# Kernel tuning notes

Hardware: AMD Instinct MI355X
Metric: run time of the kernel (lower is better)

The kernel has to match this reference:

```python
import jax, jax.numpy as jnp
import numpy as np
import math

D_MODEL = 1024
NUM_HEADS = 16
HEAD_DIM = D_MODEL // NUM_HEADS
EPS = 1e-6
ROPE_BASE = 10000.0


def _rope_cos_sin(seq_len, dim, dtype):
    inv_freq = 1.0 / (ROPE_BASE ** (jnp.arange(0, dim, 2, dtype=jnp.float32) / dim))
    t = jnp.arange(seq_len, dtype=jnp.float32)
    freqs = jnp.outer(t, inv_freq)                 # [s, dim/2]
    emb = jnp.concatenate([freqs, freqs], axis=-1)  # [s, dim]
    return jnp.cos(emb).astype(dtype), jnp.sin(emb).astype(dtype)


def _rotate_half(x):
    x1, x2 = jnp.split(x, 2, axis=-1)
    return jnp.concatenate([-x2, x1], axis=-1)


def setup_inputs() -> dict:
    key = jax.random.key(0)
    k1, k2, k3 = jax.random.split(key, 3)
    b, s = 2, 2048
    x = jax.random.normal(k1, (b, s, D_MODEL), dtype=jnp.float32)
    norm_w = jnp.ones((D_MODEL,), dtype=jnp.float32)
    qkv_w = jax.random.normal(k2, (3 * D_MODEL, D_MODEL), dtype=jnp.float32) * (1.0 / math.sqrt(D_MODEL))
    qkv_b = jnp.zeros((3 * D_MODEL,), dtype=jnp.float32)
    proj_w = jax.random.normal(k3, (D_MODEL, D_MODEL), dtype=jnp.float32) * (1.0 / math.sqrt(D_MODEL))
    proj_b = jnp.zeros((D_MODEL,), dtype=jnp.float32)
    return {"x": x, "norm_w": norm_w, "qkv_w": qkv_w, "qkv_b": qkv_b,
            "proj_w": proj_w, "proj_b": proj_b}


def reference(x, norm_w, qkv_w, qkv_b, proj_w, proj_b):
    b, s, d = x.shape
    # RMSNorm (pre-LN)
    xn = x * jax.lax.rsqrt(jnp.mean(x * x, axis=-1, keepdims=True) + EPS) * norm_w
    # Fused QKV
    qkv = jnp.einsum('bsd,ed->bse', xn, qkv_w) + qkv_b
    q, k, v = jnp.split(qkv, 3, axis=-1)
    # [b, h, s, hd]
    def shape(t):
        return t.reshape(b, s, NUM_HEADS, HEAD_DIM).transpose(0, 2, 1, 3)
    q, k, v = shape(q), shape(k), shape(v)
    # RoPE on head_dim
    cos, sin = _rope_cos_sin(s, HEAD_DIM, x.dtype)  # [s, hd]
    q = q * cos + _rotate_half(q) * sin
    k = k * cos + _rotate_half(k) * sin
    # Naive causal attention
    scale = 1.0 / math.sqrt(HEAD_DIM)
    scores = jnp.einsum('bhqd,bhkd->bhqk', q, k) * scale
    causal = jnp.tril(jnp.ones((s, s), dtype=bool))
    scores = jnp.where(causal, scores, -jnp.inf)
    attn = jax.nn.softmax(scores, axis=-1)
    y = jnp.einsum('bhqk,bhkd->bhqd', attn, v)
    y = y.transpose(0, 2, 1, 3).reshape(b, s, d)
    return jnp.einsum('bsd,ed->bse', y, proj_w) + proj_b
```

## Files before the change

### kernel.cpp

```cpp
#include <hip/hip_runtime.h>
#include <cstdint>
#include <cstddef>

#define NB 2
#define NS 2048
#define ND 1024
#define NH 16
#define HD 64
#define ROWS 4096
#define E3 3072

using bf16 = __bf16;
typedef __attribute__((ext_vector_type(4))) __bf16 bf16x4;
typedef __attribute__((ext_vector_type(8))) __bf16 bf16x8;
typedef __attribute__((ext_vector_type(4))) float f32x4;

__device__ __forceinline__ f32x4 mfma16(bf16x8 a, bf16x8 b, f32x4 c) {
    return __builtin_amdgcn_mfma_f32_16x16x32_bf16(a, b, c, 0, 0, 0);
}

__device__ __forceinline__ void gll16(const bf16* src, bf16* lds) {
    __builtin_amdgcn_global_load_lds(
        (const __attribute__((address_space(1))) void*)src,
        (__attribute__((address_space(3))) void*)lds, 16, 0, 0);
}

__global__ __launch_bounds__(256) void rope_table(float4* __restrict__ tab) {
    int idx = blockIdx.x * 256 + threadIdx.x;
    int s = idx >> 4, j = idx & 15;
    float f0 = powf(10000.0f, -(float)j * (1.0f / 32.0f));
    float f1 = powf(10000.0f, -(float)(j + 16) * (1.0f / 32.0f));
    float sn0, c0, sn1, c1;
    sincosf((float)s * f0, &sn0, &c0);
    sincosf((float)s * f1, &sn1, &c1);
    tab[idx] = make_float4(c0, sn0, c1, sn1);
}

__global__ __launch_bounds__(256) void cast_weights(const float* __restrict__ qkv_w,
                                                    const float* __restrict__ proj_w,
                                                    bf16* __restrict__ wq) {
    const int n1 = E3 * ND;
    int i = (blockIdx.x * 256 + threadIdx.x) * 4;
    const float* src = (i < n1) ? (qkv_w + i) : (proj_w + (i - n1));
    float4 v = *(const float4*)src;
    bf16x4 o;
    o[0] = (bf16)v.x; o[1] = (bf16)v.y; o[2] = (bf16)v.z; o[3] = (bf16)v.w;
    *(bf16x4*)(wq + i) = o;
}

__global__ __launch_bounds__(256) void rmsnorm_cast(const float* __restrict__ x,
                                                    const float* __restrict__ w,
                                                    bf16* __restrict__ xn) {
    int row = blockIdx.x;
    int tid = threadIdx.x;
    const float* xr = x + (size_t)row * ND;
    float4 v = ((const float4*)xr)[tid];
    float ss = v.x*v.x + v.y*v.y + v.z*v.z + v.w*v.w;
    #pragma unroll
    for (int m = 32; m >= 1; m >>= 1) ss += __shfl_xor(ss, m);
    __shared__ float wsum[4];
    if ((tid & 63) == 0) wsum[tid >> 6] = ss;
    __syncthreads();
    float total = wsum[0] + wsum[1] + wsum[2] + wsum[3];
    float scale = rsqrtf(total * (1.0f / ND) + 1e-6f);
    float4 wv = ((const float4*)w)[tid];
    bf16x4 o;
    o[0] = (bf16)(v.x * scale * wv.x);
    o[1] = (bf16)(v.y * scale * wv.y);
    o[2] = (bf16)(v.z * scale * wv.z);
    o[3] = (bf16)(v.w * scale * wv.w);
    ((bf16x4*)(xn + (size_t)row * ND))[tid] = o;
}

__global__ __launch_bounds__(256) void gemm_qkv_rope(const bf16* __restrict__ A,
                                                     const bf16* __restrict__ Bm,
                                                     const float* __restrict__ bias,
                                                     const float4* __restrict__ tab,
                                                     bf16* __restrict__ Qb,
                                                     bf16* __restrict__ Kb,
                                                     bf16* __restrict__ Vf) {
    const int K = ND;
    __shared__ bf16 Asm[128 * 32];
    __shared__ bf16 Bsm[128 * 32];
    const int tid = threadIdx.x;
    const int wave = tid >> 6, lane = tid & 63;
    const int quad = lane >> 4, l15 = lane & 15;
    const int row0 = blockIdx.x * 128, col0 = blockIdx.y * 128;
    const int wr = (wave >> 1) * 64, wc = (wave & 1) * 64;
    const int srow = lane >> 2;
    const int scol = (lane & 3) * 8;

    f32x4 acc[4][4] = {};

    for (int k0 = 0; k0 < K; k0 += 32) {
        #pragma unroll
        for (int i = 0; i < 2; ++i) {
            int r = wave * 32 + i * 16;
            gll16(A + (size_t)(row0 + r + srow) * K + k0 + scol, Asm + r * 32);
            gll16(Bm + (size_t)(col0 + r + srow) * K + k0 + scol, Bsm + r * 32);
        }
        __syncthreads();
        bf16x8 af[4], bff[4];
        #pragma unroll
        for (int t = 0; t < 4; ++t) {
            af[t]  = *(const bf16x8*)(Asm + (wr + t * 16 + l15) * 32 + quad * 8);
            bff[t] = *(const bf16x8*)(Bsm + (wc + t * 16 + l15) * 32 + quad * 8);
        }
        #pragma unroll
        for (int mt = 0; mt < 4; ++mt)
            #pragma unroll
            for (int nt = 0; nt < 4; ++nt)
                acc[mt][nt] = mfma16(af[mt], bff[nt], acc[mt][nt]);
        __syncthreads();
    }

    float bb[4];
    #pragma unroll
    for (int nt = 0; nt < 4; ++nt) bb[nt] = bias[col0 + wc + nt * 16 + l15];

    const int region = col0 >> 10;
    if (region == 2) {
        const int cv = col0 - 2048 + wc;
        const int h = cv >> 6;
        const int b = row0 >> 11;
        const int sloc = row0 & (NS - 1);
        const int kg0 = (sloc + wr) >> 5;
        bf16* vh = Vf + (size_t)(b * NH + h) * 131072;
        #pragma unroll
        for (int Gw = 0; Gw < 2; ++Gw) {
            #pragma unroll
            for (int nt = 0; nt < 4; ++nt) {
                bf16x8 vf8;
                #pragma unroll
                for (int r = 0; r < 4; ++r) {
                    vf8[r]     = (bf16)(acc[2 * Gw][nt][r] + bb[nt]);
                    vf8[4 + r] = (bf16)(acc[2 * Gw + 1][nt][r] + bb[nt]);
                }
                *(bf16x8*)(vh + ((size_t)(kg0 + Gw) * 4 + nt) * 512 + lane * 8) = vf8;
            }
        }
    } else {
        const float scale = (region == 0) ? 0.125f : 1.0f;
        bf16* Ob = (region == 0) ? Qb : Kb;
        const int h = ((col0 + wc) & 1023) >> 6;
        #pragma unroll
        for (int mt = 0; mt < 4; ++mt) {
            #pragma unroll
            for (int r = 0; r < 4; ++r) {
                int row = row0 + wr + mt * 16 + quad * 4 + r;
                int s = row & (NS - 1);
                int b = row >> 11;
                float4 cs = tab[s * 16 + l15];
                size_t obase = ((size_t)(b * NH + h) * NS + s) * 64;
                #pragma unroll
                for (int nt = 0; nt < 4; ++nt) {
                    float v  = acc[mt][nt][r] + bb[nt];
                    float vp = acc[mt][nt ^ 2][r] + bb[nt ^ 2];
                    float cc = (nt & 1) ? cs.z : cs.x;
                    float ss = (nt & 1) ? cs.w : cs.y;
                    float res = (nt < 2) ? (v * cc - vp * ss) : (v * cc + vp * ss);
                    Ob[obase + nt * 16 + l15] = (bf16)(res * scale);
                }
            }
        }
    }
}

__global__ __launch_bounds__(256) void gemm_proj(const bf16* __restrict__ A,
                                                 const bf16* __restrict__ Bm,
                                                 const float* __restrict__ bias,
                                                 float* __restrict__ C) {
    __shared__ bf16 Asm[128 * 32];
    __shared__ bf16 Bsm[64 * 32];
    const int tid = threadIdx.x;
    const int wave = tid >> 6, lane = tid & 63;
    const int quad = lane >> 4, l15 = lane & 15;
    const int row0 = blockIdx.x * 128, col0 = blockIdx.y * 64;
    const int wr = (wave >> 1) * 64, wc = (wave & 1) * 32;
    const int srow = lane >> 2;
    const int scol = (lane & 3) * 8;

    f32x4 acc[4][2] = {};

    for (int k0 = 0; k0 < ND; k0 += 32) {
        gll16(A + (size_t)(row0 + wave * 32 + srow) * ND + k0 + scol, Asm + (wave * 32) * 32);
        gll16(A + (size_t)(row0 + wave * 32 + 16 + srow) * ND + k0 + scol, Asm + (wave * 32 + 16) * 32);
        gll16(Bm + (size_t)(col0 + wave * 16 + srow) * ND + k0 + scol, Bsm + (wave * 16) * 32);
        __syncthreads();
        bf16x8 af[4], bff[2];
        #pragma unroll
        for (int t = 0; t < 4; ++t)
            af[t] = *(const bf16x8*)(Asm + (wr + t * 16 + l15) * 32 + quad * 8);
        #pragma unroll
        for (int t = 0; t < 2; ++t)
            bff[t] = *(const bf16x8*)(Bsm + (wc + t * 16 + l15) * 32 + quad * 8);
        #pragma unroll
        for (int mt = 0; mt < 4; ++mt)
            #pragma unroll
            for (int nt = 0; nt < 2; ++nt)
                acc[mt][nt] = mfma16(af[mt], bff[nt], acc[mt][nt]);
        __syncthreads();
    }

    #pragma unroll
    for (int nt = 0; nt < 2; ++nt) {
        int col = col0 + wc + nt * 16 + l15;
        float bv = bias[col];
        #pragma unroll
        for (int mt = 0; mt < 4; ++mt) {
            int row = row0 + wr + mt * 16 + quad * 4;
            #pragma unroll
            for (int r = 0; r < 4; ++r)
                C[(size_t)(row + r) * ND + col] = acc[mt][nt][r] + bv;
        }
    }
}

__global__ __launch_bounds__(256) void attn(const bf16* __restrict__ Q,
                                            const bf16* __restrict__ K,
                                            const bf16* __restrict__ Vf,
                                            bf16* __restrict__ Y) {
    __shared__ bf16 Ksm[2][8192];
    __shared__ bf16 Vsm[2][8192];
    int bid = blockIdx.x;
    int g = bid >> 5;
    int bh = bid & 31;
    int qt = (g < 8) ? (15 - g) : (g - 8);
    int tid = threadIdx.x;
    int wave = tid >> 6, lane = tid & 63;
    int quad = lane >> 4, l15 = lane & 15;
    int q0 = qt * 128 + wave * 32;
    const bf16* Qh = Q + (size_t)bh * NS * 64;
    const bf16* Kh = K + (size_t)bh * NS * 64;
    const float NEG_INF = -__builtin_inff();

    const int krow = wave * 8 + (lane >> 3);
    const int ksx  = (lane & 7) ^ (krow & 7);
    const bf16* sK = Kh + (size_t)krow * 64 + ksx * 8;
    const bf16* sV = Vf + (size_t)bh * 131072 + wave * 2048 + lane * 8;

    const bf16* pk0 = &Ksm[0][l15 * 64 + ((quad) ^ (l15 & 7)) * 8];
    const bf16* pk1 = &Ksm[0][l15 * 64 + ((4 + quad) ^ (l15 & 7)) * 8];
    const bf16* pvf = &Vsm[0][lane * 8];

    bf16x8 bq[2][2];
    #pragma unroll
    for (int t = 0; t < 2; ++t)
        #pragma unroll
        for (int hh = 0; hh < 2; ++hh)
            bq[t][hh] = *(const bf16x8*)(Qh + (size_t)(q0 + t * 16 + l15) * 64 + hh * 32 + quad * 8);

    f32x4 o[2][4] = {};
    float lsum[2] = {0.f, 0.f};

    auto stage = [&](int c, int par) {
        const int kb = c * 128;
        bf16* dK = &Ksm[par][wave * 512];
        bf16* dV = &Vsm[par][wave * 2048];
        #pragma unroll
        for (int i = 0; i < 4; ++i)
            gll16(sK + (size_t)(kb + i * 32) * 64, dK + i * 2048);
        #pragma unroll
        for (int nt = 0; nt < 4; ++nt)
            gll16(sV + (size_t)(kb >> 5) * 2048 + nt * 512, dV + nt * 512);
    };

    auto compute = [&](int cc, int par) {
        const int kb = cc * 128;
        const int pb = par * 8192;
        #pragma unroll
        for (int ksub = 0; ksub < 4; ++ksub) {
            const int kbs = kb + ksub * 32;
            if (kbs <= q0) {
                bf16x8 ak00 = *(const bf16x8*)(pk0 + pb + ksub * 2048);
                bf16x8 ak01 = *(const bf16x8*)(pk1 + pb + ksub * 2048);
                bf16x8 ak10 = *(const bf16x8*)(pk0 + pb + ksub * 2048 + 1024);
                bf16x8 ak11 = *(const bf16x8*)(pk1 + pb + ksub * 2048 + 1024);
                bf16x8 vf0 = *(const bf16x8*)(pvf + pb + ksub * 2048);
                bf16x8 vf1 = *(const bf16x8*)(pvf + pb + ksub * 2048 + 512);
                bf16x8 vf2 = *(const bf16x8*)(pvf + pb + ksub * 2048 + 1024);
                bf16x8 vf3 = *(const bf16x8*)(pvf + pb + ksub * 2048 + 1536);
                const bool masked = (kbs == q0);
                #pragma unroll
                for (int t = 0; t < 2; ++t) {
                    f32x4 sh0 = {}, sh1 = {};
                    sh0 = mfma16(ak00, bq[t][0], sh0);
                    sh0 = mfma16(ak01, bq[t][1], sh0);
                    sh1 = mfma16(ak10, bq[t][0], sh1);
                    sh1 = mfma16(ak11, bq[t][1], sh1);
                    if (masked) {
                        int qy = q0 + t * 16 + l15;
                        #pragma unroll
                        for (int r = 0; r < 4; ++r) {
                            if (kbs + quad * 4 + r > qy)      sh0[r] = NEG_INF;
                            if (kbs + 16 + quad * 4 + r > qy) sh1[r] = NEG_INF;
                        }
                    }
                    bf16x8 pa;
                    float ls = 0.f;
                    #pragma unroll
                    for (int j = 0; j < 4; ++j) {
                        float p0 = __expf(sh0[j]);
                        float p1 = __expf(sh1[j]);
                        ls += p0 + p1;
                        pa[j] = (bf16)p0;
                        pa[4 + j] = (bf16)p1;
                    }
                    lsum[t] += ls;
                    o[t][0] = mfma16(pa, vf0, o[t][0]);
                    o[t][1] = mfma16(pa, vf1, o[t][1]);
                    o[t][2] = mfma16(pa, vf2, o[t][2]);
                    o[t][3] = mfma16(pa, vf3, o[t][3]);
                }
            }
        }
    };

    const int ncb = qt + 1;
    stage(0, 0);
    __syncthreads();
    for (int c = 0; c < ncb; ++c) {
        const int par = c & 1;
        if (c + 1 < ncb) stage(c + 1, par ^ 1);
        compute(c, par);
        __syncthreads();
    }

    int b = bh >> 4, h = bh & 15;
    #pragma unroll
    for (int t = 0; t < 2; ++t) {
        float red = lsum[t];
        red += __shfl_xor(red, 16);
        red += __shfl_xor(red, 32);
        #pragma unroll
        for (int r = 0; r < 4; ++r) {
            float il = 1.0f / __shfl(red, quad * 4 + r);
            size_t row = (size_t)(b * NS + q0 + t * 16 + quad * 4 + r);
            #pragma unroll
            for (int nt = 0; nt < 4; ++nt)
                Y[row * ND + h * 64 + nt * 16 + l15] = (bf16)(o[t][nt][r] * il);
        }
    }
}

extern "C" void kernel_launch(void* const* d_in, const int* in_sizes, int n_in,
                              void* d_out, int out_size, void* d_ws, size_t ws_size,
                              hipStream_t stream) {
    const float* x      = (const float*)d_in[0];
    const float* norm_w = (const float*)d_in[1];
    const float* qkv_w  = (const float*)d_in[2];
    const float* qkv_b  = (const float*)d_in[3];
    const float* proj_w = (const float*)d_in[4];
    const float* proj_b = (const float*)d_in[5];
    float* out = (float*)d_out;

    char* ws = (char*)d_ws;
    size_t off = 0;
    bf16* xn    = (bf16*)(ws + off); off += (size_t)ROWS * ND * 2;
    bf16* wq    = (bf16*)(ws + off); off += (size_t)E3 * ND * 2;
    bf16* wp    = (bf16*)(ws + off); off += (size_t)ND * ND * 2;
    bf16* Qb    = (bf16*)(ws + off); off += (size_t)NB * NH * NS * HD * 2;
    bf16* Kb    = (bf16*)(ws + off); off += (size_t)NB * NH * NS * HD * 2;
    bf16* Vfrag = (bf16*)(ws + off); off += (size_t)NB * NH * HD * NS * 2;
    bf16* Y     = (bf16*)(ws + off); off += (size_t)ROWS * ND * 2;
    float4* tab = (float4*)(ws + off); off += (size_t)NS * 16 * sizeof(float4);

    rope_table<<<NS * 16 / 256, 256, 0, stream>>>(tab);
    cast_weights<<<(E3 * ND + ND * ND) / 1024, 256, 0, stream>>>(qkv_w, proj_w, wq);
    rmsnorm_cast<<<ROWS, 256, 0, stream>>>(x, norm_w, xn);
    gemm_qkv_rope<<<dim3(ROWS / 128, E3 / 128), 256, 0, stream>>>(xn, wq, qkv_b, tab, Qb, Kb, Vfrag);
    attn<<<NB * NH * (NS / 128), 256, 0, stream>>>(Qb, Kb, Vfrag, Y);
    gemm_proj<<<dim3(ROWS / 128, ND / 64), 256, 0, stream>>>(Y, wp, proj_b, out);
}
```

Measured before the change: 191.4 us.

## Merge prep kernels and stage Q/K and attention outputs through LDS for coalesced stores

Combines the rope table, weight cast and RMSNorm kernels into one launch with block-index branching, removing two launch gaps. The Q/K RoPE epilogue and the attention output epilogue now write per-wave tiles into shared memory, then emit 16-byte vector stores to global memory. Previously each lane wrote scattered 2-byte values. The LDS staging adds shared-memory traffic and reuses buffers that must be idle by then, relying on prior barriers and explicit waitcnts.

```diff
diff --git a/kernel.cpp b/kernel.cpp
--- a/kernel.cpp
+++ b/kernel.cpp
@@ -25,51 +25,52 @@
         (__attribute__((address_space(3))) void*)lds, 16, 0, 0);
 }
 
-__global__ __launch_bounds__(256) void rope_table(float4* __restrict__ tab) {
-    int idx = blockIdx.x * 256 + threadIdx.x;
-    int s = idx >> 4, j = idx & 15;
-    float f0 = powf(10000.0f, -(float)j * (1.0f / 32.0f));
-    float f1 = powf(10000.0f, -(float)(j + 16) * (1.0f / 32.0f));
-    float sn0, c0, sn1, c1;
-    sincosf((float)s * f0, &sn0, &c0);
-    sincosf((float)s * f1, &sn1, &c1);
-    tab[idx] = make_float4(c0, sn0, c1, sn1);
-}
-
-__global__ __launch_bounds__(256) void cast_weights(const float* __restrict__ qkv_w,
-                                                    const float* __restrict__ proj_w,
-                                                    bf16* __restrict__ wq) {
-    const int n1 = E3 * ND;
-    int i = (blockIdx.x * 256 + threadIdx.x) * 4;
-    const float* src = (i < n1) ? (qkv_w + i) : (proj_w + (i - n1));
-    float4 v = *(const float4*)src;
-    bf16x4 o;
-    o[0] = (bf16)v.x; o[1] = (bf16)v.y; o[2] = (bf16)v.z; o[3] = (bf16)v.w;
-    *(bf16x4*)(wq + i) = o;
-}
-
-__global__ __launch_bounds__(256) void rmsnorm_cast(const float* __restrict__ x,
-                                                    const float* __restrict__ w,
-                                                    bf16* __restrict__ xn) {
-    int row = blockIdx.x;
+__global__ __launch_bounds__(256) void prep(const float* __restrict__ qkv_w,
+                                            const float* __restrict__ proj_w,
+                                            const float* __restrict__ x,
+                                            const float* __restrict__ norm_w,
+                                            bf16* __restrict__ wq,
+                                            bf16* __restrict__ xn,
+                                            float4* __restrict__ tab) {
+    __shared__ float wsum[4];
+    int bid = blockIdx.x;
     int tid = threadIdx.x;
-    const float* xr = x + (size_t)row * ND;
-    float4 v = ((const float4*)xr)[tid];
-    float ss = v.x*v.x + v.y*v.y + v.z*v.z + v.w*v.w;
-    #pragma unroll
-    for (int m = 32; m >= 1; m >>= 1) ss += __shfl_xor(ss, m);
-    __shared__ float wsum[4];
-    if ((tid & 63) == 0) wsum[tid >> 6] = ss;
-    __syncthreads();
-    float total = wsum[0] + wsum[1] + wsum[2] + wsum[3];
-    float scale = rsqrtf(total * (1.0f / ND) + 1e-6f);
-    float4 wv = ((const float4*)w)[tid];
-    bf16x4 o;
-    o[0] = (bf16)(v.x * scale * wv.x);
-    o[1] = (bf16)(v.y * scale * wv.y);
-    o[2] = (bf16)(v.z * scale * wv.z);
-    o[3] = (bf16)(v.w * scale * wv.w);
-    ((bf16x4*)(xn + (size_t)row * ND))[tid] = o;
+    if (bid < 4096) {
+        const int n1 = E3 * ND;
+        int i = (bid * 256 + tid) * 4;
+        const float* src = (i < n1) ? (qkv_w + i) : (proj_w + (i - n1));
+        float4 v = *(const float4*)src;
+        bf16x4 o;
+        o[0] = (bf16)v.x; o[1] = (bf16)v.y; o[2] = (bf16)v.z; o[3] = (bf16)v.w;
+        *(bf16x4*)(wq + i) = o;
+    } else if (bid < 8192) {
+        int row = bid - 4096;
+        const float* xr = x + (size_t)row * ND;
+        float4 v = ((const float4*)xr)[tid];
+        float ss = v.x*v.x + v.y*v.y + v.z*v.z + v.w*v.w;
+        #pragma unroll
+        for (int m = 32; m >= 1; m >>= 1) ss += __shfl_xor(ss, m);
+        if ((tid & 63) == 0) wsum[tid >> 6] = ss;
+        __syncthreads();
+        float total = wsum[0] + wsum[1] + wsum[2] + wsum[3];
+        float scale = rsqrtf(total * (1.0f / ND) + 1e-6f);
+        float4 wv = ((const float4*)norm_w)[tid];
+        bf16x4 o;
+        o[0] = (bf16)(v.x * scale * wv.x);
+        o[1] = (bf16)(v.y * scale * wv.y);
+        o[2] = (bf16)(v.z * scale * wv.z);
+        o[3] = (bf16)(v.w * scale * wv.w);
+        ((bf16x4*)(xn + (size_t)row * ND))[tid] = o;
+    } else {
+        int idx = (bid - 8192) * 256 + tid;
+        int s = idx >> 4, j = idx & 15;
+        float f0 = powf(10000.0f, -(float)j * (1.0f / 32.0f));
+        float f1 = powf(10000.0f, -(float)(j + 16) * (1.0f / 32.0f));
+        float sn0, c0, sn1, c1;
+        sincosf((float)s * f0, &sn0, &c0);
+        sincosf((float)s * f1, &sn1, &c1);
+        tab[idx] = make_float4(c0, sn0, c1, sn1);
+    }
 }
 
 __global__ __launch_bounds__(256) void gemm_qkv_rope(const bf16* __restrict__ A,
@@ -80,8 +81,9 @@
                                                      bf16* __restrict__ Kb,
                                                      bf16* __restrict__ Vf) {
     const int K = ND;
-    __shared__ bf16 Asm[128 * 32];
-    __shared__ bf16 Bsm[128 * 32];
+    __shared__ bf16 smem[8192];
+    bf16* Asm = smem;
+    bf16* Bsm = smem + 4096;
     const int tid = threadIdx.x;
     const int wave = tid >> 6, lane = tid & 63;
     const int quad = lane >> 4, l15 = lane & 15;
@@ -143,25 +145,40 @@
         const float scale = (region == 0) ? 0.125f : 1.0f;
         bf16* Ob = (region == 0) ? Qb : Kb;
         const int h = ((col0 + wc) & 1023) >> 6;
-        #pragma unroll
-        for (int mt = 0; mt < 4; ++mt) {
-            #pragma unroll
-            for (int r = 0; r < 4; ++r) {
-                int row = row0 + wr + mt * 16 + quad * 4 + r;
-                int s = row & (NS - 1);
-                int b = row >> 11;
-                float4 cs = tab[s * 16 + l15];
-                size_t obase = ((size_t)(b * NH + h) * NS + s) * 64;
+        bf16* ep = smem + wave * 2048;
+        #pragma unroll
+        for (int p = 0; p < 2; ++p) {
+            #pragma unroll
+            for (int mtl = 0; mtl < 2; ++mtl) {
+                const int mt = p * 2 + mtl;
                 #pragma unroll
-                for (int nt = 0; nt < 4; ++nt) {
-                    float v  = acc[mt][nt][r] + bb[nt];
-                    float vp = acc[mt][nt ^ 2][r] + bb[nt ^ 2];
-                    float cc = (nt & 1) ? cs.z : cs.x;
-                    float ss = (nt & 1) ? cs.w : cs.y;
-                    float res = (nt < 2) ? (v * cc - vp * ss) : (v * cc + vp * ss);
-                    Ob[obase + nt * 16 + l15] = (bf16)(res * scale);
+                for (int r = 0; r < 4; ++r) {
+                    int row = row0 + wr + mt * 16 + quad * 4 + r;
+                    int s = row & (NS - 1);
+                    float4 cs = tab[s * 16 + l15];
+                    #pragma unroll
+                    for (int nt = 0; nt < 4; ++nt) {
+                        float v  = acc[mt][nt][r] + bb[nt];
+                        float vp = acc[mt][nt ^ 2][r] + bb[nt ^ 2];
+                        float cc = (nt & 1) ? cs.z : cs.x;
+                        float ss = (nt & 1) ? cs.w : cs.y;
+                        float res = (nt < 2) ? (v * cc - vp * ss) : (v * cc + vp * ss);
+                        ep[(mtl * 16 + quad * 4 + r) * 64 + nt * 16 + l15] = (bf16)(res * scale);
+                    }
                 }
             }
+            asm volatile("s_waitcnt lgkmcnt(0)" ::: "memory");
+            const int rowp = row0 + wr + p * 32;
+            const int b = rowp >> 11;
+            const int s0p = rowp & (NS - 1);
+            bf16* gbase = Ob + ((size_t)(b * NH + h) * NS + s0p + (lane >> 3)) * 64 + (lane & 7) * 8;
+            const bf16* lbase = ep + (lane >> 3) * 64 + (lane & 7) * 8;
+            #pragma unroll
+            for (int i = 0; i < 4; ++i) {
+                bf16x8 v8 = *(const bf16x8*)(lbase + i * 512);
+                *(bf16x8*)(gbase + (size_t)i * 512) = v8;
+            }
+            asm volatile("s_waitcnt lgkmcnt(0)" ::: "memory");
         }
     }
 }
@@ -327,6 +344,7 @@
     }
 
     int b = bh >> 4, h = bh & 15;
+    bf16* ep = &Ksm[0][wave * 2048];
     #pragma unroll
     for (int t = 0; t < 2; ++t) {
         float red = lsum[t];
@@ -335,11 +353,18 @@
         #pragma unroll
         for (int r = 0; r < 4; ++r) {
             float il = 1.0f / __shfl(red, quad * 4 + r);
-            size_t row = (size_t)(b * NS + q0 + t * 16 + quad * 4 + r);
             #pragma unroll
             for (int nt = 0; nt < 4; ++nt)
-                Y[row * ND + h * 64 + nt * 16 + l15] = (bf16)(o[t][nt][r] * il);
-        }
+                ep[(t * 16 + quad * 4 + r) * 64 + nt * 16 + l15] = (bf16)(o[t][nt][r] * il);
+        }
+    }
+    asm volatile("s_waitcnt lgkmcnt(0)" ::: "memory");
+    bf16* gbase = Y + ((size_t)(b * NS + q0 + (lane >> 3)) << 10) + h * 64 + (lane & 7) * 8;
+    const bf16* lbase = ep + (lane >> 3) * 64 + (lane & 7) * 8;
+    #pragma unroll
+    for (int i = 0; i < 4; ++i) {
+        bf16x8 v8 = *(const bf16x8*)(lbase + i * 512);
+        *(bf16x8*)(gbase + ((size_t)i * 8 << 10)) = v8;
     }
 }
 
@@ -365,9 +390,7 @@
     bf16* Y     = (bf16*)(ws + off); off += (size_t)ROWS * ND * 2;
     float4* tab = (float4*)(ws + off); off += (size_t)NS * 16 * sizeof(float4);
 
-    rope_table<<<NS * 16 / 256, 256, 0, stream>>>(tab);
-    cast_weights<<<(E3 * ND + ND * ND) / 1024, 256, 0, stream>>>(qkv_w, proj_w, wq);
-    rmsnorm_cast<<<ROWS, 256, 0, stream>>>(x, norm_w, xn);
+    prep<<<8320, 256, 0, stream>>>(qkv_w, proj_w, x, norm_w, wq, xn, tab);
     gemm_qkv_rope<<<dim3(ROWS / 128, E3 / 128), 256, 0, stream>>>(xn, wq, qkv_b, tab, Qb, Kb, Vfrag);
     attn<<<NB * NH * (NS / 128), 256, 0, stream>>>(Qb, Kb, Vfrag, Y);
     gemm_proj<<<dim3(ROWS / 128, ND / 64), 256, 0, stream>>>(Y, wp, proj_b, out);
```

Result: no change. 189.4 us (-1.0%).
